# Kernel optimization log

Measured on AMD Instinct MI355X. Metric: run time of the kernel, lower is better.

## Reference

```python
import jax, jax.numpy as jnp
import numpy as np

LAMBDA_REG = 0.1
RHO = 1.0

B_VOXELS = 4096   # batch of voxels
M_MEAS = 256      # measurements per voxel
K_ATOMS = 512     # dictionary atoms


def setup_inputs() -> dict:
    key = jax.random.key(0)
    k1, k2 = jax.random.split(key)
    # data: [voxels, measurements] as passed to fit()
    Y = jax.random.normal(k1, (B_VOXELS, M_MEAS), dtype=jnp.float32)
    # dictionary matrix Phi: [measurements, atoms]; kernels are nonnegative signals
    A = jax.random.uniform(k2, (M_MEAS, K_ATOMS), dtype=jnp.float32)
    return {"Y": Y, "A": A, "max_iter": 30}


def _soft_threshold(v, t):
    # L1Norm().prox
    return jnp.sign(v) * jnp.maximum(jnp.abs(v) - t, 0.0)


def reference(Y, A, max_iter):
    """ADMM solve: min_x ||Y^T - A x||^2 + lambda*||x||_1  s.t. x >= 0.
    Returns X_hat with shape [voxels, atoms]."""
    Yb = Y.T                                    # [M, B]
    K = A.shape[1]
    AtY = A.T @ Yb                              # [K, B]
    LHS = A.T @ A + RHO * jnp.eye(K, dtype=A.dtype)
    c_and_lower = jax.scipy.linalg.cho_factor(LHS)

    x0 = jnp.zeros_like(AtY)
    z0 = jnp.zeros_like(AtY)
    u0 = jnp.zeros_like(AtY)

    def admm_step(carry, _):
        x, z, u = carry
        rhs = AtY + RHO * (z - u)
        x_new = jax.scipy.linalg.cho_solve(c_and_lower, rhs)
        v = x_new + u
        v_proj = jnp.maximum(v, 0.0)            # nonnegativity prox (constrained=True)
        z_new = _soft_threshold(v_proj, LAMBDA_REG / RHO)  # L1 prox (lambda_reg>0)
        u_new = u + x_new - z_new
        return (x_new, z_new, u_new), None

    (X_hat, _, _), _ = jax.lax.scan(admm_step, (x0, z0, u0), None, length=max_iter)
    return X_hat.T                              # [voxels, atoms]
```

## Files before the change

### kernel.cpp

```cpp
#include <hip/hip_runtime.h>

#define NVOX   4096
#define NMEAS  256
#define NATOMS 512
#define NITER  30

typedef __attribute__((ext_vector_type(8))) short s8v;
typedef __attribute__((ext_vector_type(4))) short s4v;
typedef __attribute__((ext_vector_type(4))) float f32x4;

__device__ __forceinline__ unsigned short f2bf(float x) {
    unsigned u = __builtin_bit_cast(unsigned, x);
    u += 0x7fff + ((u >> 16) & 1);
    return (unsigned short)(u >> 16);
}
__device__ __forceinline__ float bf2f(unsigned short b) {
    unsigned u = ((unsigned)b) << 16;
    return __builtin_bit_cast(float, u);
}
__device__ __forceinline__ float g_of(float v) {
    return fmaxf(v - 0.1f, 0.0f) - fminf(v, 0.1f);
}

__global__ __launch_bounds__(256) void g_kernel_d(const float* __restrict__ A,
                                                  double* __restrict__ Gd,
                                                  float* __restrict__ Gf) {
    __shared__ float arow[NATOMS];
    int i = blockIdx.x;
    for (int k = threadIdx.x; k < NATOMS; k += 256) arow[k] = A[i * NATOMS + k];
    __syncthreads();
    int j = threadIdx.x;
    const float* aj = A + j * NATOMS;
    double s = (i == j) ? 1.0 : 0.0;
#pragma unroll 4
    for (int k = 0; k < NATOMS; ++k) s += (double)arow[k] * (double)aj[k];
    Gd[i * NMEAS + j] = s;
    Gf[i * NMEAS + j] = (float)s;
}

__global__ __launch_bounds__(1024) void sweep_inverse(const float* __restrict__ src,
                                                      float* __restrict__ dst) {
    __shared__ float s_dn[NMEAS];
    __shared__ float s_dt[NMEAS];
    int t = threadIdx.x;
    int rb = t & 31;
    int cb = t >> 5;
    float vals[8][8];
#pragma unroll
    for (int i = 0; i < 8; ++i) {
        const float* row = &src[(8 * rb + i) * NMEAS + 8 * cb];
        float4 a = *(const float4*)row;
        float4 b = *(const float4*)(row + 4);
        vals[i][0] = a.x; vals[i][1] = a.y; vals[i][2] = a.z; vals[i][3] = a.w;
        vals[i][4] = b.x; vals[i][5] = b.y; vals[i][6] = b.z; vals[i][7] = b.w;
    }
#pragma unroll 1
    for (int p = 0; p < NMEAS; ++p) {
        int pb = p >> 3, pi = p & 7;
        __syncthreads();
        if (cb == pb) {
#pragma unroll
            for (int i = 0; i < 8; ++i) {
                float v = vals[i][0];
#pragma unroll
                for (int j = 1; j < 8; ++j) if (pi == j) v = vals[i][j];
                s_dn[8 * rb + i] = v;
                s_dt[i * 32 + rb] = v;
            }
        }
        __syncthreads();
        float d   = s_dn[p];
        float inv = 1.0f / d;
        float rv[8], cv[8];
#pragma unroll
        for (int i = 0; i < 8; ++i) rv[i] = s_dt[i * 32 + rb];
#pragma unroll
        for (int j = 0; j < 8; ++j) cv[j] = s_dn[8 * cb + j] * inv;
#pragma unroll
        for (int i = 0; i < 8; ++i)
#pragma unroll
            for (int j = 0; j < 8; ++j) vals[i][j] -= rv[i] * cv[j];
        if (rb == pb) {
#pragma unroll
            for (int i = 0; i < 8; ++i) if (pi == i) {
#pragma unroll
                for (int j = 0; j < 8; ++j) vals[i][j] = cv[j];
            }
        }
        if (cb == pb) {
#pragma unroll
            for (int j = 0; j < 8; ++j) if (pi == j) {
#pragma unroll
                for (int i = 0; i < 8; ++i)
                    vals[i][j] = (rb == pb && pi == i) ? -inv : rv[i] * inv;
            }
        }
    }
#pragma unroll
    for (int i = 0; i < 8; ++i)
#pragma unroll
        for (int j = 0; j < 8; ++j)
            dst[(8 * rb + i) * NMEAS + 8 * cb + j] = -vals[i][j];
}

template <typename TB>
__global__ __launch_bounds__(256) void mm_gd(const double* __restrict__ Gd,
                                             const TB* __restrict__ X,
                                             double* __restrict__ P) {
    __shared__ __align__(16) double row[NMEAS];
    int i = blockIdx.x;
    row[threadIdx.x] = Gd[i * NMEAS + threadIdx.x];
    __syncthreads();
    int j = threadIdx.x;
    double s = 0.0;
#pragma unroll 4
    for (int k = 0; k < NMEAS; ++k) s += row[k] * (double)X[k * NMEAS + j];
    P[i * NMEAS + j] = s;
}

template <typename TB>
__global__ __launch_bounds__(256) void upd_newton(const TB* __restrict__ X,
                                                  const double* __restrict__ P,
                                                  double* __restrict__ Xn) {
    __shared__ __align__(16) double row[NMEAS];
    int i = blockIdx.x;
    row[threadIdx.x] = (double)X[i * NMEAS + threadIdx.x];
    __syncthreads();
    int j = threadIdx.x;
    double s = 0.0;
#pragma unroll 4
    for (int k = 0; k < NMEAS; ++k) s += row[k] * P[k * NMEAS + j];
    Xn[i * NMEAS + j] = 2.0 * row[j] - s;
}

__global__ __launch_bounds__(256) void h_kernel_d(const double* __restrict__ Gi,
                                                  const float* __restrict__ A,
                                                  double* __restrict__ H) {
    __shared__ __align__(16) double grow[NMEAS];
    int i = blockIdx.x;
    grow[threadIdx.x] = Gi[i * NMEAS + threadIdx.x];
    __syncthreads();
    int k0 = threadIdx.x;
    double s0 = 0.0, s1 = 0.0;
#pragma unroll 4
    for (int j = 0; j < NMEAS; ++j) {
        double g = grow[j];
        s0 += g * (double)A[j * NATOMS + k0];
        s1 += g * (double)A[j * NATOMS + k0 + 256];
    }
    H[i * NATOMS + k0] = s0;
    H[i * NATOMS + k0 + 256] = s1;
}

__global__ __launch_bounds__(256) void w_kernel_d(const float* __restrict__ A,
                                                  const double* __restrict__ H,
                                                  unsigned short* __restrict__ Whg,
                                                  unsigned short* __restrict__ Wlg) {
    __shared__ __align__(16) double acol[NMEAS];
    int p = blockIdx.x;
    acol[threadIdx.x] = (double)A[threadIdx.x * NATOMS + p];
    __syncthreads();
    int q0 = threadIdx.x;
    double s0 = 0.0, s1 = 0.0;
#pragma unroll 4
    for (int m = 0; m < NMEAS; ++m) {
        double a = acol[m];
        s0 += a * H[m * NATOMS + q0];
        s1 += a * H[m * NATOMS + q0 + 256];
    }
    double w0 = ((p == q0)       ? 1.0 : 0.0) - s0;
    double w1 = ((p == q0 + 256) ? 1.0 : 0.0) - s1;
    unsigned short h0 = f2bf((float)w0), h1 = f2bf((float)w1);
    Whg[p * NATOMS + q0]       = h0;
    Wlg[p * NATOMS + q0]       = f2bf((float)(w0 - (double)bf2f(h0)));
    Whg[p * NATOMS + q0 + 256] = h1;
    Wlg[p * NATOMS + q0 + 256] = f2bf((float)(w1 - (double)bf2f(h1)));
}

__global__ __launch_bounds__(256) void aty_kernel(const float* __restrict__ A,
                                                  const float* __restrict__ Y,
                                                  unsigned short* __restrict__ Dh0,
                                                  unsigned short* __restrict__ Dl0) {
    __shared__ __align__(16) float At[64][65];
    __shared__ __align__(16) float Yt[64][65];
    int b0 = blockIdx.x * 64, k0 = blockIdx.y * 64;
    int t = threadIdx.x, tx = t & 15, ty = t >> 4;
    float acc[4][4] = {};
    for (int m0 = 0; m0 < NMEAS; m0 += 64) {
        __syncthreads();
        {
            int kk = t & 63, mr = t >> 6;
#pragma unroll
            for (int p = 0; p < 16; ++p)
                At[mr + 4 * p][kk] = A[(m0 + mr + 4 * p) * NATOMS + k0 + kk];
            int mm = t & 63, br = t >> 6;
#pragma unroll
            for (int p = 0; p < 16; ++p)
                Yt[mm][br + 4 * p] = Y[(b0 + br + 4 * p) * NMEAS + m0 + mm];
        }
        __syncthreads();
#pragma unroll 4
        for (int m = 0; m < 64; ++m) {
            float av[4], yv[4];
#pragma unroll
            for (int i = 0; i < 4; ++i) av[i] = At[m][ty * 4 + i];
#pragma unroll
            for (int j = 0; j < 4; ++j) yv[j] = Yt[m][tx * 4 + j];
#pragma unroll
            for (int i = 0; i < 4; ++i)
#pragma unroll
                for (int j = 0; j < 4; ++j) acc[i][j] += av[i] * yv[j];
        }
    }
#pragma unroll
    for (int j = 0; j < 4; ++j) {
        int b = b0 + tx * 4 + j;
        s4v h4, l4;
#pragma unroll
        for (int i = 0; i < 4; ++i) {
            float f = acc[i][j];
            unsigned short h = f2bf(f);
            h4[i] = (short)h;
            l4[i] = (short)f2bf(f - bf2f(h));
        }
        *(s4v*)&Dh0[(long)b * NATOMS + k0 + ty * 4] = h4;
        *(s4v*)&Dl0[(long)b * NATOMS + k0 + ty * 4] = l4;
    }
}

template <int FIRST, int LAST>
__global__ __launch_bounds__(256) void admm_delta(
        const unsigned short* __restrict__ Whg,
        const unsigned short* __restrict__ Wlg,
        const unsigned short* __restrict__ Dhg,
        const unsigned short* __restrict__ Dlg,
        float* __restrict__ xbuf,
        float* __restrict__ vbuf,
        unsigned short* __restrict__ DhOut,
        unsigned short* __restrict__ DlOut,
        float* __restrict__ out) {
    __shared__ __align__(16) char smem[30720];
    unsigned short* Whs = (unsigned short*)smem;
    unsigned short* Wls = Whs + 2 * 64 * 40;
    unsigned short* Dhs = Wls + 2 * 64 * 40;
    unsigned short* Dls = Dhs + 2 * 32 * 40;

    const int t = threadIdx.x;
    const int lane = t & 63, wv = t >> 6;
    const int ln = lane & 15, kg = lane >> 4;

    int bid = blockIdx.x + (blockIdx.y << 7);
    int xr = bid & 7, q = bid >> 3;
    int bx = xr * 16 + (q >> 3);
    int by = q & 7;
    const int n0 = bx * 32, m0 = by * 64;

    const int wm = t >> 2, wslot = t & 3;
    const int dn = (t & 127) >> 2, dslot = t & 3;
    const unsigned short* Dg  = (t < 128) ? Dhg : Dlg;
    unsigned short*       Dsb = (t < 128) ? Dhs : Dls;

    f32x4 acc[2] = {};
    s8v rwh, rwl, rd;

#define GLOAD(kc)                                                             \
    {                                                                         \
        long ko = (long)(kc)*32;                                              \
        rwh = *(const s8v*)&Whg[(long)(m0 + wm) * NATOMS + ko + wslot * 8];   \
        rwl = *(const s8v*)&Wlg[(long)(m0 + wm) * NATOMS + ko + wslot * 8];   \
        rd  = *(const s8v*)&Dg [(long)(n0 + dn) * NATOMS + ko + dslot * 8];   \
    }
#define DSWRITE(b)                                                  \
    {                                                               \
        *(s8v*)&Whs[(b)*2560 + wm * 40 + wslot * 8] = rwh;          \
        *(s8v*)&Wls[(b)*2560 + wm * 40 + wslot * 8] = rwl;          \
        *(s8v*)&Dsb[(b)*1280 + dn * 40 + dslot * 8] = rd;           \
    }

    GLOAD(0);
    DSWRITE(0);
#pragma unroll 1
    for (int c = 0; c < 16; ++c) {
        if (c < 15) GLOAD(c + 1);
        __syncthreads();
        const int b = c & 1;
        const unsigned short* wh = &Whs[b * 2560];
        const unsigned short* wl = &Wls[b * 2560];
        const unsigned short* dh = &Dhs[b * 1280];
        const unsigned short* dl = &Dls[b * 1280];
        s8v ah, al, bh[2], bl[2];
        {
            int row = wv * 16 + ln;
            ah = *(const s8v*)&wh[row * 40 + kg * 8];
            al = *(const s8v*)&wl[row * 40 + kg * 8];
        }
#pragma unroll
        for (int ni = 0; ni < 2; ++ni) {
            int row = ni * 16 + ln;
            bh[ni] = *(const s8v*)&dh[row * 40 + kg * 8];
            bl[ni] = *(const s8v*)&dl[row * 40 + kg * 8];
        }
#pragma unroll
        for (int ni = 0; ni < 2; ++ni) {
            acc[ni] = __builtin_amdgcn_mfma_f32_16x16x32_bf16(ah, bh[ni], acc[ni], 0, 0, 0);
            acc[ni] = __builtin_amdgcn_mfma_f32_16x16x32_bf16(ah, bl[ni], acc[ni], 0, 0, 0);
            acc[ni] = __builtin_amdgcn_mfma_f32_16x16x32_bf16(al, bh[ni], acc[ni], 0, 0, 0);
        }
        if (c < 15) DSWRITE((c + 1) & 1);
    }
#undef GLOAD
#undef DSWRITE

    __syncthreads();
    float* xT = (float*)smem;

    if (!LAST) {
#pragma unroll
        for (int ni = 0; ni < 2; ++ni) {
            int nn = n0 + ni * 16 + ln;
            f32x4 dlt;
#pragma unroll
            for (int j = 0; j < 4; ++j) {
                int m = m0 + wv * 16 + kg * 4 + j;
                long idx = (long)m * NVOX + nn;
                float dx = acc[ni][j];
                float xn, vn, gold;
                if (FIRST) {
                    xn = dx; vn = xn; gold = 0.0f;
                } else {
                    xn = xbuf[idx] + dx;
                    float vp = vbuf[idx];
                    vn = xn + fminf(vp, 0.1f);
                    gold = g_of(vp);
                }
                xbuf[idx] = xn;
                vbuf[idx] = vn;
                dlt[j] = g_of(vn) - gold;
            }
            int nl = ni * 16 + ln;
            int ml = wv * 16 + kg * 4;
            *(f32x4*)&xT[nl * 68 + ml] = dlt;
        }
        __syncthreads();
        int nl = t >> 3, seg = t & 7;
        {
            s8v hv, lv;
#pragma unroll
            for (int e = 0; e < 8; ++e) {
                float f = xT[nl * 68 + seg * 8 + e];
                unsigned short h = f2bf(f);
                hv[e] = (short)h;
                lv[e] = (short)f2bf(f - bf2f(h));
            }
            *(s8v*)&DhOut[(long)(n0 + nl) * NATOMS + m0 + seg * 8] = hv;
            *(s8v*)&DlOut[(long)(n0 + nl) * NATOMS + m0 + seg * 8] = lv;
        }
    } else {
#pragma unroll
        for (int ni = 0; ni < 2; ++ni) {
            int nn = n0 + ni * 16 + ln;
            f32x4 tv;
#pragma unroll
            for (int j = 0; j < 4; ++j) {
                int m = m0 + wv * 16 + kg * 4 + j;
                tv[j] = xbuf[(long)m * NVOX + nn] + acc[ni][j];
            }
            int nl = ni * 16 + ln;
            int ml = wv * 16 + kg * 4;
            *(f32x4*)&xT[nl * 68 + ml] = tv;
        }
        __syncthreads();
        int nl = t >> 3, seg = t & 7;
#pragma unroll
        for (int qq = 0; qq < 2; ++qq) {
            f32x4 v = *(const f32x4*)&xT[nl * 68 + seg * 8 + qq * 4];
            *(f32x4*)&out[(long)(n0 + nl) * NATOMS + m0 + seg * 8 + qq * 4] = v;
        }
    }
}

extern "C" void kernel_launch(void* const* d_in, const int* in_sizes, int n_in,
                              void* d_out, int out_size, void* d_ws, size_t ws_size,
                              hipStream_t stream) {
    const float* Y = (const float*)d_in[0];
    const float* A = (const float*)d_in[1];

    float* ws = (float*)d_ws;
    double* Gd  = (double*)(ws + 0);
    float*  Gf  = ws + 131072;
    float*  X0f = ws + 196608;
    double* X1d = (double*)(ws + 262144);
    double* Pd  = (double*)(ws + 393216);
    double* X2d = (double*)(ws + 131072);
    double* Hd  = (double*)(ws + 393216);
    float*  xbuf = ws + 655360;
    unsigned short* Whg = (unsigned short*)(ws + 0);
    unsigned short* Wlg = (unsigned short*)(ws + 131072);
    unsigned short* DAh = (unsigned short*)(ws + 2752512);
    unsigned short* DAl = (unsigned short*)(ws + 3801088);
    unsigned short* DBh = (unsigned short*)(ws + 4849664);
    unsigned short* DBl = (unsigned short*)(ws + 5898240);
    float* vbuf = (float*)d_out;
    float* outp = (float*)d_out;

    g_kernel_d<<<256, 256, 0, stream>>>(A, Gd, Gf);
    sweep_inverse<<<1, 1024, 0, stream>>>(Gf, X0f);
    mm_gd<float><<<256, 256, 0, stream>>>(Gd, X0f, Pd);
    upd_newton<float><<<256, 256, 0, stream>>>(X0f, Pd, X1d);
    mm_gd<double><<<256, 256, 0, stream>>>(Gd, X1d, Pd);
    upd_newton<double><<<256, 256, 0, stream>>>(X1d, Pd, X2d);
    h_kernel_d<<<256, 256, 0, stream>>>(X2d, A, Hd);
    w_kernel_d<<<512, 256, 0, stream>>>(A, Hd, Whg, Wlg);
    aty_kernel<<<dim3(64, 8), 256, 0, stream>>>(A, Y, DAh, DAl);

    dim3 ig(NVOX / 32, NATOMS / 64);
    unsigned short *ch = DAh, *cl = DAl, *nh = DBh, *nl = DBl;
    admm_delta<1, 0><<<ig, 256, 0, stream>>>(Whg, Wlg, ch, cl, xbuf, vbuf, nh, nl, nullptr);
    { unsigned short* s; s = ch; ch = nh; nh = s; s = cl; cl = nl; nl = s; }
    for (int it = 2; it <= NITER - 1; ++it) {
        admm_delta<0, 0><<<ig, 256, 0, stream>>>(Whg, Wlg, ch, cl, xbuf, vbuf, nh, nl, nullptr);
        unsigned short* s; s = ch; ch = nh; nh = s; s = cl; cl = nl; nl = s;
    }
    admm_delta<0, 1><<<ig, 256, 0, stream>>>(Whg, Wlg, ch, cl, xbuf, vbuf, nullptr, nullptr, outp);
}
```

Measured before the change: 1.006 ms.

## Fuse all ADMM iterations into one persistent kernel keeping state in registers

Replaces the 30 separate admm_delta launches with a single kernel where each 512-thread block owns 32 voxels across all 512 atoms. The x and v state stays in registers and the per-iteration delta is kept in LDS, which removes the global round trips for xbuf, vbuf and the D buffers as well as the launch overhead. The W matrices are now read straight from global/L2 on every iteration with no LDS staging. Only 128 blocks are launched, which may underfill the 256 CUs, and register pressure is high.

```diff
diff --git a/kernel.cpp b/kernel.cpp
--- a/kernel.cpp
+++ b/kernel.cpp
@@ -228,155 +228,89 @@
     }
 }
 
-template <int FIRST, int LAST>
-__global__ __launch_bounds__(256) void admm_delta(
+__global__ __launch_bounds__(512) void admm_fused(
         const unsigned short* __restrict__ Whg,
         const unsigned short* __restrict__ Wlg,
-        const unsigned short* __restrict__ Dhg,
-        const unsigned short* __restrict__ Dlg,
-        float* __restrict__ xbuf,
-        float* __restrict__ vbuf,
-        unsigned short* __restrict__ DhOut,
-        unsigned short* __restrict__ DlOut,
+        const unsigned short* __restrict__ D0h,
+        const unsigned short* __restrict__ D0l,
         float* __restrict__ out) {
-    __shared__ __align__(16) char smem[30720];
-    unsigned short* Whs = (unsigned short*)smem;
-    unsigned short* Wls = Whs + 2 * 64 * 40;
-    unsigned short* Dhs = Wls + 2 * 64 * 40;
-    unsigned short* Dls = Dhs + 2 * 32 * 40;
+    __shared__ __align__(16) unsigned short Dh[32][520];
+    __shared__ __align__(16) unsigned short Dl[32][520];
 
     const int t = threadIdx.x;
     const int lane = t & 63, wv = t >> 6;
     const int ln = lane & 15, kg = lane >> 4;
-
-    int bid = blockIdx.x + (blockIdx.y << 7);
-    int xr = bid & 7, q = bid >> 3;
-    int bx = xr * 16 + (q >> 3);
-    int by = q & 7;
-    const int n0 = bx * 32, m0 = by * 64;
-
-    const int wm = t >> 2, wslot = t & 3;
-    const int dn = (t & 127) >> 2, dslot = t & 3;
-    const unsigned short* Dg  = (t < 128) ? Dhg : Dlg;
-    unsigned short*       Dsb = (t < 128) ? Dhs : Dls;
-
-    f32x4 acc[2] = {};
-    s8v rwh, rwl, rd;
-
-#define GLOAD(kc)                                                             \
-    {                                                                         \
-        long ko = (long)(kc)*32;                                              \
-        rwh = *(const s8v*)&Whg[(long)(m0 + wm) * NATOMS + ko + wslot * 8];   \
-        rwl = *(const s8v*)&Wlg[(long)(m0 + wm) * NATOMS + ko + wslot * 8];   \
-        rd  = *(const s8v*)&Dg [(long)(n0 + dn) * NATOMS + ko + dslot * 8];   \
-    }
-#define DSWRITE(b)                                                  \
-    {                                                               \
-        *(s8v*)&Whs[(b)*2560 + wm * 40 + wslot * 8] = rwh;          \
-        *(s8v*)&Wls[(b)*2560 + wm * 40 + wslot * 8] = rwl;          \
-        *(s8v*)&Dsb[(b)*1280 + dn * 40 + dslot * 8] = rd;           \
-    }
-
-    GLOAD(0);
-    DSWRITE(0);
+    const long vb = (long)blockIdx.x * 32;
+
+    f32x4 xacc[4][2] = {};
+    f32x4 vreg[4][2] = {};
+
 #pragma unroll 1
-    for (int c = 0; c < 16; ++c) {
-        if (c < 15) GLOAD(c + 1);
-        __syncthreads();
-        const int b = c & 1;
-        const unsigned short* wh = &Whs[b * 2560];
-        const unsigned short* wl = &Wls[b * 2560];
-        const unsigned short* dh = &Dhs[b * 1280];
-        const unsigned short* dl = &Dls[b * 1280];
-        s8v ah, al, bh[2], bl[2];
-        {
-            int row = wv * 16 + ln;
-            ah = *(const s8v*)&wh[row * 40 + kg * 8];
-            al = *(const s8v*)&wl[row * 40 + kg * 8];
-        }
-#pragma unroll
-        for (int ni = 0; ni < 2; ++ni) {
-            int row = ni * 16 + ln;
-            bh[ni] = *(const s8v*)&dh[row * 40 + kg * 8];
-            bl[ni] = *(const s8v*)&dl[row * 40 + kg * 8];
-        }
-#pragma unroll
-        for (int ni = 0; ni < 2; ++ni) {
-            acc[ni] = __builtin_amdgcn_mfma_f32_16x16x32_bf16(ah, bh[ni], acc[ni], 0, 0, 0);
-            acc[ni] = __builtin_amdgcn_mfma_f32_16x16x32_bf16(ah, bl[ni], acc[ni], 0, 0, 0);
-            acc[ni] = __builtin_amdgcn_mfma_f32_16x16x32_bf16(al, bh[ni], acc[ni], 0, 0, 0);
-        }
-        if (c < 15) DSWRITE((c + 1) & 1);
-    }
-#undef GLOAD
-#undef DSWRITE
-
-    __syncthreads();
-    float* xT = (float*)smem;
-
-    if (!LAST) {
-#pragma unroll
-        for (int ni = 0; ni < 2; ++ni) {
-            int nn = n0 + ni * 16 + ln;
-            f32x4 dlt;
-#pragma unroll
-            for (int j = 0; j < 4; ++j) {
-                int m = m0 + wv * 16 + kg * 4 + j;
-                long idx = (long)m * NVOX + nn;
-                float dx = acc[ni][j];
-                float xn, vn, gold;
-                if (FIRST) {
-                    xn = dx; vn = xn; gold = 0.0f;
-                } else {
-                    xn = xbuf[idx] + dx;
-                    float vp = vbuf[idx];
-                    vn = xn + fminf(vp, 0.1f);
-                    gold = g_of(vp);
+    for (int it = 0; it < NITER; ++it) {
+#pragma unroll 1
+        for (int kc = 0; kc < 16; ++kc) {
+            const int ko = kc * 32 + kg * 8;
+            s8v bh[2], bl[2];
+            if (it == 0) {
+#pragma unroll
+                for (int nt = 0; nt < 2; ++nt) {
+                    long r = (vb + nt * 16 + ln) * NATOMS + ko;
+                    bh[nt] = *(const s8v*)&D0h[r];
+                    bl[nt] = *(const s8v*)&D0l[r];
                 }
-                xbuf[idx] = xn;
-                vbuf[idx] = vn;
-                dlt[j] = g_of(vn) - gold;
-            }
-            int nl = ni * 16 + ln;
-            int ml = wv * 16 + kg * 4;
-            *(f32x4*)&xT[nl * 68 + ml] = dlt;
-        }
-        __syncthreads();
-        int nl = t >> 3, seg = t & 7;
-        {
-            s8v hv, lv;
-#pragma unroll
-            for (int e = 0; e < 8; ++e) {
-                float f = xT[nl * 68 + seg * 8 + e];
-                unsigned short h = f2bf(f);
-                hv[e] = (short)h;
-                lv[e] = (short)f2bf(f - bf2f(h));
-            }
-            *(s8v*)&DhOut[(long)(n0 + nl) * NATOMS + m0 + seg * 8] = hv;
-            *(s8v*)&DlOut[(long)(n0 + nl) * NATOMS + m0 + seg * 8] = lv;
-        }
-    } else {
-#pragma unroll
-        for (int ni = 0; ni < 2; ++ni) {
-            int nn = n0 + ni * 16 + ln;
-            f32x4 tv;
-#pragma unroll
-            for (int j = 0; j < 4; ++j) {
-                int m = m0 + wv * 16 + kg * 4 + j;
-                tv[j] = xbuf[(long)m * NVOX + nn] + acc[ni][j];
-            }
-            int nl = ni * 16 + ln;
-            int ml = wv * 16 + kg * 4;
-            *(f32x4*)&xT[nl * 68 + ml] = tv;
-        }
-        __syncthreads();
-        int nl = t >> 3, seg = t & 7;
-#pragma unroll
-        for (int qq = 0; qq < 2; ++qq) {
-            f32x4 v = *(const f32x4*)&xT[nl * 68 + seg * 8 + qq * 4];
-            *(f32x4*)&out[(long)(n0 + nl) * NATOMS + m0 + seg * 8 + qq * 4] = v;
-        }
-    }
+            } else {
+#pragma unroll
+                for (int nt = 0; nt < 2; ++nt) {
+                    bh[nt] = *(const s8v*)&Dh[nt * 16 + ln][ko];
+                    bl[nt] = *(const s8v*)&Dl[nt * 16 + ln][ko];
+                }
+            }
+#pragma unroll
+            for (int mt = 0; mt < 4; ++mt) {
+                const long mrow = (long)((wv * 4 + mt) * 16 + ln) * NATOMS + ko;
+                s8v ah = *(const s8v*)&Whg[mrow];
+                s8v al = *(const s8v*)&Wlg[mrow];
+#pragma unroll
+                for (int nt = 0; nt < 2; ++nt) {
+                    xacc[mt][nt] = __builtin_amdgcn_mfma_f32_16x16x32_bf16(ah, bh[nt], xacc[mt][nt], 0, 0, 0);
+                    xacc[mt][nt] = __builtin_amdgcn_mfma_f32_16x16x32_bf16(ah, bl[nt], xacc[mt][nt], 0, 0, 0);
+                    xacc[mt][nt] = __builtin_amdgcn_mfma_f32_16x16x32_bf16(al, bh[nt], xacc[mt][nt], 0, 0, 0);
+                }
+            }
+        }
+        if (it == NITER - 1) break;
+        __syncthreads();
+#pragma unroll
+        for (int mt = 0; mt < 4; ++mt)
+#pragma unroll
+            for (int nt = 0; nt < 2; ++nt) {
+                s4v h4, l4;
+#pragma unroll
+                for (int j = 0; j < 4; ++j) {
+                    float xv = xacc[mt][nt][j];
+                    float vp = vreg[mt][nt][j];
+                    float vn = xv + fminf(vp, 0.1f);
+                    float dlt = g_of(vn) - g_of(vp);
+                    vreg[mt][nt][j] = vn;
+                    unsigned short h = f2bf(dlt);
+                    h4[j] = (short)h;
+                    l4[j] = (short)f2bf(dlt - bf2f(h));
+                }
+                int nl = nt * 16 + ln;
+                int m  = (wv * 4 + mt) * 16 + kg * 4;
+                *(s4v*)&Dh[nl][m] = h4;
+                *(s4v*)&Dl[nl][m] = l4;
+            }
+        __syncthreads();
+    }
+#pragma unroll
+    for (int mt = 0; mt < 4; ++mt)
+#pragma unroll
+        for (int nt = 0; nt < 2; ++nt) {
+            long n = vb + nt * 16 + ln;
+            int  m = (wv * 4 + mt) * 16 + kg * 4;
+            *(f32x4*)&out[n * NATOMS + m] = xacc[mt][nt];
+        }
 }
 
 extern "C" void kernel_launch(void* const* d_in, const int* in_sizes, int n_in,
@@ -393,14 +327,10 @@
     double* Pd  = (double*)(ws + 393216);
     double* X2d = (double*)(ws + 131072);
     double* Hd  = (double*)(ws + 393216);
-    float*  xbuf = ws + 655360;
     unsigned short* Whg = (unsigned short*)(ws + 0);
     unsigned short* Wlg = (unsigned short*)(ws + 131072);
     unsigned short* DAh = (unsigned short*)(ws + 2752512);
     unsigned short* DAl = (unsigned short*)(ws + 3801088);
-    unsigned short* DBh = (unsigned short*)(ws + 4849664);
-    unsigned short* DBl = (unsigned short*)(ws + 5898240);
-    float* vbuf = (float*)d_out;
     float* outp = (float*)d_out;
 
     g_kernel_d<<<256, 256, 0, stream>>>(A, Gd, Gf);
@@ -413,13 +343,5 @@
     w_kernel_d<<<512, 256, 0, stream>>>(A, Hd, Whg, Wlg);
     aty_kernel<<<dim3(64, 8), 256, 0, stream>>>(A, Y, DAh, DAl);
 
-    dim3 ig(NVOX / 32, NATOMS / 64);
-    unsigned short *ch = DAh, *cl = DAl, *nh = DBh, *nl = DBl;
-    admm_delta<1, 0><<<ig, 256, 0, stream>>>(Whg, Wlg, ch, cl, xbuf, vbuf, nh, nl, nullptr);
-    { unsigned short* s; s = ch; ch = nh; nh = s; s = cl; cl = nl; nl = s; }
-    for (int it = 2; it <= NITER - 1; ++it) {
-        admm_delta<0, 0><<<ig, 256, 0, stream>>>(Whg, Wlg, ch, cl, xbuf, vbuf, nh, nl, nullptr);
-        unsigned short* s; s = ch; ch = nh; nh = s; s = cl; cl = nl; nl = s;
-    }
-    admm_delta<0, 1><<<ig, 256, 0, stream>>>(Whg, Wlg, ch, cl, xbuf, vbuf, nullptr, nullptr, outp);
-}
+    admm_fused<<<128, 512, 0, stream>>>(Whg, Wlg, DAh, DAl, outp);
+}
```

Measured after the change: 1.372 ms. 36.4% more time.

## Widen ADMM tile to 64 voxels and store state voxel-major without LDS transpose

Applied to the files above, without the earlier changes.

Each block of the iterative ADMM kernel now covers 64 voxels × 64 atoms instead of 32 × 64. Each wave reuses one voxel fragment across four atom sub-tiles, which halves the grid and the number of times the W operand is reloaded. The x/v state buffers move from atom-major to voxel-major layout. That lets each thread update and write its accumulator values directly with vector stores, dropping the LDS transpose staging and two barriers. The cost is more LDS and registers per block and fewer blocks to fill the GPU.

```diff
diff --git a/kernel.cpp b/kernel.cpp
--- a/kernel.cpp
+++ b/kernel.cpp
@@ -239,42 +239,42 @@
         unsigned short* __restrict__ DhOut,
         unsigned short* __restrict__ DlOut,
         float* __restrict__ out) {
-    __shared__ __align__(16) char smem[30720];
+    __shared__ __align__(16) char smem[40960];
     unsigned short* Whs = (unsigned short*)smem;
     unsigned short* Wls = Whs + 2 * 64 * 40;
     unsigned short* Dhs = Wls + 2 * 64 * 40;
-    unsigned short* Dls = Dhs + 2 * 32 * 40;
+    unsigned short* Dls = Dhs + 2 * 64 * 40;
 
     const int t = threadIdx.x;
     const int lane = t & 63, wv = t >> 6;
     const int ln = lane & 15, kg = lane >> 4;
 
-    int bid = blockIdx.x + (blockIdx.y << 7);
+    int bid = blockIdx.x + (blockIdx.y << 6);
     int xr = bid & 7, q = bid >> 3;
-    int bx = xr * 16 + (q >> 3);
+    int bx = xr * 8 + (q >> 3);
     int by = q & 7;
-    const int n0 = bx * 32, m0 = by * 64;
+    const int n0 = bx * 64, m0 = by * 64;
 
     const int wm = t >> 2, wslot = t & 3;
-    const int dn = (t & 127) >> 2, dslot = t & 3;
-    const unsigned short* Dg  = (t < 128) ? Dhg : Dlg;
-    unsigned short*       Dsb = (t < 128) ? Dhs : Dls;
-
-    f32x4 acc[2] = {};
-    s8v rwh, rwl, rd;
+    const int tn = t >> 2, tslot = t & 3;
+
+    f32x4 acc[4] = {};
+    s8v rwh, rwl, rth, rtl;
 
 #define GLOAD(kc)                                                             \
     {                                                                         \
         long ko = (long)(kc)*32;                                              \
         rwh = *(const s8v*)&Whg[(long)(m0 + wm) * NATOMS + ko + wslot * 8];   \
         rwl = *(const s8v*)&Wlg[(long)(m0 + wm) * NATOMS + ko + wslot * 8];   \
-        rd  = *(const s8v*)&Dg [(long)(n0 + dn) * NATOMS + ko + dslot * 8];   \
+        rth = *(const s8v*)&Dhg[(long)(n0 + tn) * NATOMS + ko + tslot * 8];   \
+        rtl = *(const s8v*)&Dlg[(long)(n0 + tn) * NATOMS + ko + tslot * 8];   \
     }
 #define DSWRITE(b)                                                  \
     {                                                               \
         *(s8v*)&Whs[(b)*2560 + wm * 40 + wslot * 8] = rwh;          \
         *(s8v*)&Wls[(b)*2560 + wm * 40 + wslot * 8] = rwl;          \
-        *(s8v*)&Dsb[(b)*1280 + dn * 40 + dslot * 8] = rd;           \
+        *(s8v*)&Dhs[(b)*2560 + tn * 40 + tslot * 8] = rth;          \
+        *(s8v*)&Dls[(b)*2560 + tn * 40 + tslot * 8] = rtl;          \
     }
 
     GLOAD(0);
@@ -286,95 +286,73 @@
         const int b = c & 1;
         const unsigned short* wh = &Whs[b * 2560];
         const unsigned short* wl = &Wls[b * 2560];
-        const unsigned short* dh = &Dhs[b * 1280];
-        const unsigned short* dl = &Dls[b * 1280];
-        s8v ah, al, bh[2], bl[2];
+        const unsigned short* dh = &Dhs[b * 2560];
+        const unsigned short* dl = &Dls[b * 2560];
+        s8v ah[4], al[4], bh, bl;
+#pragma unroll
+        for (int mi = 0; mi < 4; ++mi) {
+            ah[mi] = *(const s8v*)&wh[(mi * 16 + ln) * 40 + kg * 8];
+            al[mi] = *(const s8v*)&wl[(mi * 16 + ln) * 40 + kg * 8];
+        }
         {
-            int row = wv * 16 + ln;
-            ah = *(const s8v*)&wh[row * 40 + kg * 8];
-            al = *(const s8v*)&wl[row * 40 + kg * 8];
-        }
-#pragma unroll
-        for (int ni = 0; ni < 2; ++ni) {
-            int row = ni * 16 + ln;
-            bh[ni] = *(const s8v*)&dh[row * 40 + kg * 8];
-            bl[ni] = *(const s8v*)&dl[row * 40 + kg * 8];
-        }
-#pragma unroll
-        for (int ni = 0; ni < 2; ++ni) {
-            acc[ni] = __builtin_amdgcn_mfma_f32_16x16x32_bf16(ah, bh[ni], acc[ni], 0, 0, 0);
-            acc[ni] = __builtin_amdgcn_mfma_f32_16x16x32_bf16(ah, bl[ni], acc[ni], 0, 0, 0);
-            acc[ni] = __builtin_amdgcn_mfma_f32_16x16x32_bf16(al, bh[ni], acc[ni], 0, 0, 0);
+            int r = wv * 16 + ln;
+            bh = *(const s8v*)&dh[r * 40 + kg * 8];
+            bl = *(const s8v*)&dl[r * 40 + kg * 8];
+        }
+#pragma unroll
+        for (int mi = 0; mi < 4; ++mi) {
+            acc[mi] = __builtin_amdgcn_mfma_f32_16x16x32_bf16(ah[mi], bh, acc[mi], 0, 0, 0);
+            acc[mi] = __builtin_amdgcn_mfma_f32_16x16x32_bf16(ah[mi], bl, acc[mi], 0, 0, 0);
+            acc[mi] = __builtin_amdgcn_mfma_f32_16x16x32_bf16(al[mi], bh, acc[mi], 0, 0, 0);
         }
         if (c < 15) DSWRITE((c + 1) & 1);
     }
 #undef GLOAD
 #undef DSWRITE
 
-    __syncthreads();
-    float* xT = (float*)smem;
-
+    const long nn = n0 + wv * 16 + ln;
     if (!LAST) {
 #pragma unroll
-        for (int ni = 0; ni < 2; ++ni) {
-            int nn = n0 + ni * 16 + ln;
-            f32x4 dlt;
+        for (int mi = 0; mi < 4; ++mi) {
+            long base = nn * NATOMS + m0 + mi * 16 + kg * 4;
+            f32x4 xo, vo;
+            if (!FIRST) {
+                xo = *(const f32x4*)&xbuf[base];
+                vo = *(const f32x4*)&vbuf[base];
+            }
+            f32x4 xn, vn;
+            s4v h4, l4;
 #pragma unroll
             for (int j = 0; j < 4; ++j) {
-                int m = m0 + wv * 16 + kg * 4 + j;
-                long idx = (long)m * NVOX + nn;
-                float dx = acc[ni][j];
-                float xn, vn, gold;
+                float dx = acc[mi][j];
+                float x, vnj, gold;
                 if (FIRST) {
-                    xn = dx; vn = xn; gold = 0.0f;
+                    x = dx; vnj = x; gold = 0.0f;
                 } else {
-                    xn = xbuf[idx] + dx;
-                    float vp = vbuf[idx];
-                    vn = xn + fminf(vp, 0.1f);
-                    gold = g_of(vp);
+                    x = xo[j] + dx;
+                    vnj = x + fminf(vo[j], 0.1f);
+                    gold = g_of(vo[j]);
                 }
-                xbuf[idx] = xn;
-                vbuf[idx] = vn;
-                dlt[j] = g_of(vn) - gold;
+                float dlt = g_of(vnj) - gold;
+                xn[j] = x; vn[j] = vnj;
+                unsigned short h = f2bf(dlt);
+                h4[j] = (short)h;
+                l4[j] = (short)f2bf(dlt - bf2f(h));
             }
-            int nl = ni * 16 + ln;
-            int ml = wv * 16 + kg * 4;
-            *(f32x4*)&xT[nl * 68 + ml] = dlt;
-        }
-        __syncthreads();
-        int nl = t >> 3, seg = t & 7;
-        {
-            s8v hv, lv;
-#pragma unroll
-            for (int e = 0; e < 8; ++e) {
-                float f = xT[nl * 68 + seg * 8 + e];
-                unsigned short h = f2bf(f);
-                hv[e] = (short)h;
-                lv[e] = (short)f2bf(f - bf2f(h));
-            }
-            *(s8v*)&DhOut[(long)(n0 + nl) * NATOMS + m0 + seg * 8] = hv;
-            *(s8v*)&DlOut[(long)(n0 + nl) * NATOMS + m0 + seg * 8] = lv;
+            *(f32x4*)&xbuf[base] = xn;
+            *(f32x4*)&vbuf[base] = vn;
+            *(s4v*)&DhOut[base] = h4;
+            *(s4v*)&DlOut[base] = l4;
         }
     } else {
 #pragma unroll
-        for (int ni = 0; ni < 2; ++ni) {
-            int nn = n0 + ni * 16 + ln;
-            f32x4 tv;
-#pragma unroll
-            for (int j = 0; j < 4; ++j) {
-                int m = m0 + wv * 16 + kg * 4 + j;
-                tv[j] = xbuf[(long)m * NVOX + nn] + acc[ni][j];
-            }
-            int nl = ni * 16 + ln;
-            int ml = wv * 16 + kg * 4;
-            *(f32x4*)&xT[nl * 68 + ml] = tv;
-        }
-        __syncthreads();
-        int nl = t >> 3, seg = t & 7;
-#pragma unroll
-        for (int qq = 0; qq < 2; ++qq) {
-            f32x4 v = *(const f32x4*)&xT[nl * 68 + seg * 8 + qq * 4];
-            *(f32x4*)&out[(long)(n0 + nl) * NATOMS + m0 + seg * 8 + qq * 4] = v;
+        for (int mi = 0; mi < 4; ++mi) {
+            long base = nn * NATOMS + m0 + mi * 16 + kg * 4;
+            f32x4 xo = *(const f32x4*)&xbuf[base];
+            f32x4 r;
+#pragma unroll
+            for (int j = 0; j < 4; ++j) r[j] = xo[j] + acc[mi][j];
+            *(f32x4*)&out[base] = r;
         }
     }
 }
@@ -413,7 +391,7 @@
     w_kernel_d<<<512, 256, 0, stream>>>(A, Hd, Whg, Wlg);
     aty_kernel<<<dim3(64, 8), 256, 0, stream>>>(A, Y, DAh, DAl);
 
-    dim3 ig(NVOX / 32, NATOMS / 64);
+    dim3 ig(NVOX / 64, NATOMS / 64);
     unsigned short *ch = DAh, *cl = DAl, *nh = DBh, *nl = DBl;
     admm_delta<1, 0><<<ig, 256, 0, stream>>>(Whg, Wlg, ch, cl, xbuf, vbuf, nh, nl, nullptr);
     { unsigned short* s; s = ch; ch = nh; nh = s; s = cl; cl = nl; nl = s; }
```

New measurement: 1.005 ms. Within noise of the previous version (-0.1%).
